# Kernel optimization log

Hardware: AMD Instinct MI355X
Metric: run time of the kernel (lower is better)

The kernel has to match this reference:

```python
import jax, jax.numpy as jnp
import numpy as np

N, DIM, EMB = 8192, 128, 16
WIDTHS = [64, 32, 16]


def setup_inputs() -> dict:
    key = jax.random.key(0)
    ks = jax.random.split(key, 16)
    x = jax.random.normal(ks[0], (N, DIM), dtype=jnp.float32)
    dims = [DIM] + WIDTHS + [EMB]  # 128 -> 64 -> 32 -> 16 -> 16
    params = {}
    for i in range(4):
        fan_in, fan_out = dims[i], dims[i + 1]
        params[f"W{i+1}"] = jax.random.normal(ks[1 + 2 * i], (fan_in, fan_out), dtype=jnp.float32) * (1.0 / np.sqrt(fan_in))
        params[f"b{i+1}"] = jax.random.normal(ks[2 + 2 * i], (fan_out,), dtype=jnp.float32) * 0.01
    return {"x": x, **params}


def _encode(x, W1, b1, W2, b2, W3, b3, W4, b4):
    h = jax.nn.relu(x @ W1 + b1)
    h = jax.nn.relu(h @ W2 + b2)
    h = jax.nn.relu(h @ W3 + b3)
    return h @ W4 + b4  # [N, EMB]


def _tstudent_probs(z):
    # squared euclidean distances via the norm trick (avoids [N,N,EMB] tensor)
    sq = jnp.sum(z * z, axis=1)  # [N]
    dist = jnp.maximum(sq[:, None] + sq[None, :] - 2.0 * (z @ z.T), 0.0)  # [N,N]
    numerator = 1.0 / (1.0 + dist)
    return numerator / jnp.sum(numerator, axis=1, keepdims=True)


def reference(x, W1, b1, W2, b2, W3, b3, W4, b4):
    z = _encode(x, W1, b1, W2, b2, W3, b3, W4, b4)
    return _tstudent_probs(z)
```

## Files before the change

### kernel.cpp

```cpp
#include <hip/hip_runtime.h>

#define N 8192
#define DIM 128
#define NCHUNK 32

__global__ __launch_bounds__(64) void encoder_kernel(
    const float* __restrict__ x,
    const float* __restrict__ W1, const float* __restrict__ b1,
    const float* __restrict__ W2, const float* __restrict__ b2,
    const float* __restrict__ W3, const float* __restrict__ b3,
    const float* __restrict__ W4, const float* __restrict__ b4,
    float* __restrict__ z, float* __restrict__ sqout)
{
    __shared__ float sW2[64 * 32];
    __shared__ float sW3[32 * 16];
    __shared__ float sW4[16 * 16];
    __shared__ float sb1[64];
    __shared__ float sb2[32];
    __shared__ float sb3[16];
    __shared__ float sb4[16];
    __shared__ float sW1[128 * 64];
    __shared__ float sh1[64 * 65];

    int t = threadIdx.x;
    float* sh2 = sW1;
    float* sh3 = sW1 + 2112;

    for (int idx = t; idx < 128 * 64; idx += 64) sW1[idx] = W1[idx];
    for (int idx = t; idx < 64 * 32; idx += 64) sW2[idx] = W2[idx];
    for (int idx = t; idx < 32 * 16; idx += 64) sW3[idx] = W3[idx];
    for (int idx = t; idx < 16 * 16; idx += 64) sW4[idx] = W4[idx];
    sb1[t] = b1[t];
    if (t < 32) sb2[t] = b2[t];
    if (t < 16) { sb3[t] = b3[t]; sb4[t] = b4[t]; }
    __syncthreads();

    int row = blockIdx.x * 64 + t;
    const float4* xr = (const float4*)(x + (size_t)row * DIM);

    float h1[64];
    #pragma unroll
    for (int k = 0; k < 64; ++k) h1[k] = sb1[k];
    for (int j4 = 0; j4 < 32; ++j4) {
        float4 xv = xr[j4];
        const float* w0 = &sW1[(j4 * 4 + 0) * 64];
        const float* w1 = &sW1[(j4 * 4 + 1) * 64];
        const float* w2 = &sW1[(j4 * 4 + 2) * 64];
        const float* w3 = &sW1[(j4 * 4 + 3) * 64];
        #pragma unroll
        for (int k = 0; k < 64; ++k) h1[k] = fmaf(xv.x, w0[k], h1[k]);
        #pragma unroll
        for (int k = 0; k < 64; ++k) h1[k] = fmaf(xv.y, w1[k], h1[k]);
        #pragma unroll
        for (int k = 0; k < 64; ++k) h1[k] = fmaf(xv.z, w2[k], h1[k]);
        #pragma unroll
        for (int k = 0; k < 64; ++k) h1[k] = fmaf(xv.w, w3[k], h1[k]);
    }
    #pragma unroll
    for (int k = 0; k < 64; ++k) sh1[t * 65 + k] = fmaxf(h1[k], 0.0f);

    float h2[32];
    #pragma unroll
    for (int k = 0; k < 32; ++k) h2[k] = sb2[k];
    for (int j = 0; j < 64; ++j) {
        float a = sh1[t * 65 + j];
        #pragma unroll
        for (int k = 0; k < 32; ++k) h2[k] = fmaf(a, sW2[j * 32 + k], h2[k]);
    }
    #pragma unroll
    for (int k = 0; k < 32; ++k) sh2[t * 33 + k] = fmaxf(h2[k], 0.0f);

    float h3[16];
    #pragma unroll
    for (int k = 0; k < 16; ++k) h3[k] = sb3[k];
    for (int j = 0; j < 32; ++j) {
        float a = sh2[t * 33 + j];
        #pragma unroll
        for (int k = 0; k < 16; ++k) h3[k] = fmaf(a, sW3[j * 16 + k], h3[k]);
    }
    #pragma unroll
    for (int k = 0; k < 16; ++k) sh3[t * 17 + k] = fmaxf(h3[k], 0.0f);

    float zo[16];
    #pragma unroll
    for (int k = 0; k < 16; ++k) zo[k] = sb4[k];
    for (int j = 0; j < 16; ++j) {
        float a = sh3[t * 17 + j];
        #pragma unroll
        for (int k = 0; k < 16; ++k) zo[k] = fmaf(a, sW4[j * 16 + k], zo[k]);
    }

    float s = 0.0f;
    #pragma unroll
    for (int k = 0; k < 16; ++k) s = fmaf(zo[k], zo[k], s);
    sqout[row] = s;
    float4* zr = (float4*)(z + (size_t)row * 16);
    zr[0] = make_float4(zo[0], zo[1], zo[2], zo[3]);
    zr[1] = make_float4(zo[4], zo[5], zo[6], zo[7]);
    zr[2] = make_float4(zo[8], zo[9], zo[10], zo[11]);
    zr[3] = make_float4(zo[12], zo[13], zo[14], zo[15]);
}

__global__ __launch_bounds__(256) void pass1_kernel(
    const float* __restrict__ z, const float* __restrict__ sq,
    float* __restrict__ partial)
{
    __shared__ float s_zj[256 * 16];
    __shared__ float s_sqj[256];

    int t = threadIdx.x;
    int i0 = blockIdx.x * 256 + t;
    int i1 = i0 + 4096;
    int jb = blockIdx.y * 256;

    {
        const float4* src = (const float4*)(z + (size_t)(jb + t) * 16);
        float4* dst = (float4*)(s_zj + t * 16);
        dst[0] = src[0]; dst[1] = src[1]; dst[2] = src[2]; dst[3] = src[3];
        s_sqj[t] = sq[jb + t];
    }

    float zi0[16], zi1[16];
    {
        const float4* p0 = (const float4*)(z + (size_t)i0 * 16);
        const float4* p1 = (const float4*)(z + (size_t)i1 * 16);
        #pragma unroll
        for (int q = 0; q < 4; ++q) {
            float4 v0 = p0[q]; float4 v1 = p1[q];
            zi0[4*q] = v0.x; zi0[4*q+1] = v0.y; zi0[4*q+2] = v0.z; zi0[4*q+3] = v0.w;
            zi1[4*q] = v1.x; zi1[4*q+1] = v1.y; zi1[4*q+2] = v1.z; zi1[4*q+3] = v1.w;
        }
    }
    float sqi0 = sq[i0], sqi1 = sq[i1];
    __syncthreads();

    float acc0 = 0.0f, acc1 = 0.0f;
    #pragma unroll 4
    for (int jj = 0; jj < 256; ++jj) {
        const float* zj = s_zj + jj * 16;
        float d0 = 0.0f, d1 = 0.0f;
        #pragma unroll
        for (int k = 0; k < 16; ++k) {
            float w = zj[k];
            d0 = fmaf(zi0[k], w, d0);
            d1 = fmaf(zi1[k], w, d1);
        }
        float sj = s_sqj[jj];
        float dist0 = fmaxf(fmaf(-2.0f, d0, sqi0 + sj), 0.0f);
        float dist1 = fmaxf(fmaf(-2.0f, d1, sqi1 + sj), 0.0f);
        acc0 += __builtin_amdgcn_rcpf(1.0f + dist0);
        acc1 += __builtin_amdgcn_rcpf(1.0f + dist1);
    }
    partial[blockIdx.y * N + i0] = acc0;
    partial[blockIdx.y * N + i1] = acc1;
}

__global__ __launch_bounds__(256) void pass2_kernel(
    const float* __restrict__ z, const float* __restrict__ sq,
    const float* __restrict__ partial, float* __restrict__ out)
{
    __shared__ float s_zi[16 * 16];
    __shared__ float s_sqi[16];
    __shared__ float s_inv[16];
    __shared__ float s_red[16 * NCHUNK];

    int t = threadIdx.x;
    int ibase = blockIdx.x * 16;

    s_zi[t] = z[(size_t)ibase * 16 + t];
    if (t < 16) s_sqi[t] = sq[ibase + t];
    for (int q = t; q < 16 * NCHUNK; q += 256) {
        int ii = q >> 5;
        int c  = q & (NCHUNK - 1);
        s_red[ii * NCHUNK + c] = partial[(size_t)c * N + ibase + ii];
    }
    __syncthreads();
    if (t < 16) {
        float s = 0.0f;
        #pragma unroll
        for (int c = 0; c < NCHUNK; ++c) s += s_red[t * NCHUNK + c];
        s_inv[t] = 1.0f / s;
    }
    __syncthreads();

    for (int jb = 0; jb < N; jb += 256) {
        int j = jb + t;
        float zj[16];
        {
            const float4* zp = (const float4*)(z + (size_t)j * 16);
            #pragma unroll
            for (int q = 0; q < 4; ++q) {
                float4 v = zp[q];
                zj[4*q] = v.x; zj[4*q+1] = v.y; zj[4*q+2] = v.z; zj[4*q+3] = v.w;
            }
        }
        float sqj = sq[j];
        #pragma unroll
        for (int ii = 0; ii < 16; ++ii) {
            const float* zi = s_zi + ii * 16;
            float d = 0.0f;
            #pragma unroll
            for (int k = 0; k < 16; ++k) d = fmaf(zi[k], zj[k], d);
            float dist = fmaxf(fmaf(-2.0f, d, s_sqi[ii] + sqj), 0.0f);
            float num = __builtin_amdgcn_rcpf(1.0f + dist);
            __builtin_nontemporal_store(num * s_inv[ii],
                                        &out[(size_t)(ibase + ii) * N + j]);
        }
    }
}

extern "C" void kernel_launch(void* const* d_in, const int* in_sizes, int n_in,
                              void* d_out, int out_size, void* d_ws, size_t ws_size,
                              hipStream_t stream) {
    const float* x  = (const float*)d_in[0];
    const float* W1 = (const float*)d_in[1];
    const float* b1 = (const float*)d_in[2];
    const float* W2 = (const float*)d_in[3];
    const float* b2 = (const float*)d_in[4];
    const float* W3 = (const float*)d_in[5];
    const float* b3 = (const float*)d_in[6];
    const float* W4 = (const float*)d_in[7];
    const float* b4 = (const float*)d_in[8];
    float* out = (float*)d_out;

    float* ws = (float*)d_ws;
    float* z       = ws;
    float* sq      = ws + N * 16;
    float* partial = ws + N * 16 + N;

    encoder_kernel<<<128, 64, 0, stream>>>(x, W1, b1, W2, b2, W3, b3, W4, b4, z, sq);
    pass1_kernel<<<dim3(16, NCHUNK), 256, 0, stream>>>(z, sq, partial);
    pass2_kernel<<<N / 16, 256, 0, stream>>>(z, sq, partial, out);
}
```

Before: 395.4 us.

## Pack z, norms and inverse row sums into one record and use broadcast reads

The encoder now writes each z row together with its squared norm into a 32-float packed record. A separate reduce kernel stores the inverse row sum into that same record. Pass1 and pass2 drop shared-memory staging: each thread holds one row's vector in registers and loops over the other rows, reading them through wave-uniform broadcast global loads. In pass2 each thread now writes one column across 512 rows, so each store is a coalesced row segment; the price is heavy reliance on cache for the broadcast loads and an extra kernel launch.

```diff
diff --git a/kernel.cpp b/kernel.cpp
--- a/kernel.cpp
+++ b/kernel.cpp
@@ -2,7 +2,8 @@
 
 #define N 8192
 #define DIM 128
-#define NCHUNK 32
+#define PACK 32
+#define P1_JCHUNK 16
 
 __global__ __launch_bounds__(64) void encoder_kernel(
     const float* __restrict__ x,
@@ -10,7 +11,7 @@
     const float* __restrict__ W2, const float* __restrict__ b2,
     const float* __restrict__ W3, const float* __restrict__ b3,
     const float* __restrict__ W4, const float* __restrict__ b4,
-    float* __restrict__ z, float* __restrict__ sqout)
+    float* __restrict__ packed)
 {
     __shared__ float sW2[64 * 32];
     __shared__ float sW3[32 * 16];
@@ -93,119 +94,89 @@
     float s = 0.0f;
     #pragma unroll
     for (int k = 0; k < 16; ++k) s = fmaf(zo[k], zo[k], s);
-    sqout[row] = s;
-    float4* zr = (float4*)(z + (size_t)row * 16);
-    zr[0] = make_float4(zo[0], zo[1], zo[2], zo[3]);
-    zr[1] = make_float4(zo[4], zo[5], zo[6], zo[7]);
-    zr[2] = make_float4(zo[8], zo[9], zo[10], zo[11]);
-    zr[3] = make_float4(zo[12], zo[13], zo[14], zo[15]);
+
+    float* pr = packed + (size_t)row * PACK;
+    float4* pv = (float4*)pr;
+    pv[0] = make_float4(zo[0], zo[1], zo[2], zo[3]);
+    pv[1] = make_float4(zo[4], zo[5], zo[6], zo[7]);
+    pv[2] = make_float4(zo[8], zo[9], zo[10], zo[11]);
+    pv[3] = make_float4(zo[12], zo[13], zo[14], zo[15]);
+    pr[16] = s;
 }
 
 __global__ __launch_bounds__(256) void pass1_kernel(
-    const float* __restrict__ z, const float* __restrict__ sq,
-    float* __restrict__ partial)
-{
-    __shared__ float s_zj[256 * 16];
-    __shared__ float s_sqj[256];
-
+    const float* __restrict__ packed, float* __restrict__ partial)
+{
     int t = threadIdx.x;
-    int i0 = blockIdx.x * 256 + t;
-    int i1 = i0 + 4096;
-    int jb = blockIdx.y * 256;
-
+    int i = blockIdx.x * 256 + t;
+    const int JPB = N / P1_JCHUNK;
+    int jb = blockIdx.y * JPB;
+
+    float zi[16];
+    float sqi;
     {
-        const float4* src = (const float4*)(z + (size_t)(jb + t) * 16);
-        float4* dst = (float4*)(s_zj + t * 16);
-        dst[0] = src[0]; dst[1] = src[1]; dst[2] = src[2]; dst[3] = src[3];
-        s_sqj[t] = sq[jb + t];
-    }
-
-    float zi0[16], zi1[16];
+        const float4* p = (const float4*)(packed + (size_t)i * PACK);
+        #pragma unroll
+        for (int q = 0; q < 4; ++q) {
+            float4 v = p[q];
+            zi[4*q] = v.x; zi[4*q+1] = v.y; zi[4*q+2] = v.z; zi[4*q+3] = v.w;
+        }
+        sqi = packed[(size_t)i * PACK + 16];
+    }
+
+    float acc = 0.0f;
+    const float* pr = packed + (size_t)jb * PACK;
+    #pragma unroll 2
+    for (int j = 0; j < JPB; ++j, pr += PACK) {
+        float d = 0.0f;
+        #pragma unroll
+        for (int k = 0; k < 16; ++k) d = fmaf(pr[k], zi[k], d);
+        float dist = fmaxf(fmaf(-2.0f, d, sqi + pr[16]), 0.0f);
+        acc += __builtin_amdgcn_rcpf(1.0f + dist);
+    }
+    partial[(size_t)blockIdx.y * N + i] = acc;
+}
+
+__global__ __launch_bounds__(256) void reduce_kernel(
+    const float* __restrict__ partial, float* __restrict__ packed)
+{
+    int i = blockIdx.x * 256 + threadIdx.x;
+    float s = 0.0f;
+    #pragma unroll
+    for (int c = 0; c < P1_JCHUNK; ++c) s += partial[(size_t)c * N + i];
+    packed[(size_t)i * PACK + 17] = 1.0f / s;
+}
+
+__global__ __launch_bounds__(256) void pass2_kernel(
+    const float* __restrict__ packed, float* __restrict__ out)
+{
+    int t = threadIdx.x;
+    int j = blockIdx.x * 256 + t;
+    const int IPB = N / 16;
+    int i0 = blockIdx.y * IPB;
+
+    float zj[16];
+    float sqj;
     {
-        const float4* p0 = (const float4*)(z + (size_t)i0 * 16);
-        const float4* p1 = (const float4*)(z + (size_t)i1 * 16);
+        const float4* p = (const float4*)(packed + (size_t)j * PACK);
         #pragma unroll
         for (int q = 0; q < 4; ++q) {
-            float4 v0 = p0[q]; float4 v1 = p1[q];
-            zi0[4*q] = v0.x; zi0[4*q+1] = v0.y; zi0[4*q+2] = v0.z; zi0[4*q+3] = v0.w;
-            zi1[4*q] = v1.x; zi1[4*q+1] = v1.y; zi1[4*q+2] = v1.z; zi1[4*q+3] = v1.w;
+            float4 v = p[q];
+            zj[4*q] = v.x; zj[4*q+1] = v.y; zj[4*q+2] = v.z; zj[4*q+3] = v.w;
         }
-    }
-    float sqi0 = sq[i0], sqi1 = sq[i1];
-    __syncthreads();
-
-    float acc0 = 0.0f, acc1 = 0.0f;
-    #pragma unroll 4
-    for (int jj = 0; jj < 256; ++jj) {
-        const float* zj = s_zj + jj * 16;
-        float d0 = 0.0f, d1 = 0.0f;
-        #pragma unroll
-        for (int k = 0; k < 16; ++k) {
-            float w = zj[k];
-            d0 = fmaf(zi0[k], w, d0);
-            d1 = fmaf(zi1[k], w, d1);
-        }
-        float sj = s_sqj[jj];
-        float dist0 = fmaxf(fmaf(-2.0f, d0, sqi0 + sj), 0.0f);
-        float dist1 = fmaxf(fmaf(-2.0f, d1, sqi1 + sj), 0.0f);
-        acc0 += __builtin_amdgcn_rcpf(1.0f + dist0);
-        acc1 += __builtin_amdgcn_rcpf(1.0f + dist1);
-    }
-    partial[blockIdx.y * N + i0] = acc0;
-    partial[blockIdx.y * N + i1] = acc1;
-}
-
-__global__ __launch_bounds__(256) void pass2_kernel(
-    const float* __restrict__ z, const float* __restrict__ sq,
-    const float* __restrict__ partial, float* __restrict__ out)
-{
-    __shared__ float s_zi[16 * 16];
-    __shared__ float s_sqi[16];
-    __shared__ float s_inv[16];
-    __shared__ float s_red[16 * NCHUNK];
-
-    int t = threadIdx.x;
-    int ibase = blockIdx.x * 16;
-
-    s_zi[t] = z[(size_t)ibase * 16 + t];
-    if (t < 16) s_sqi[t] = sq[ibase + t];
-    for (int q = t; q < 16 * NCHUNK; q += 256) {
-        int ii = q >> 5;
-        int c  = q & (NCHUNK - 1);
-        s_red[ii * NCHUNK + c] = partial[(size_t)c * N + ibase + ii];
-    }
-    __syncthreads();
-    if (t < 16) {
-        float s = 0.0f;
-        #pragma unroll
-        for (int c = 0; c < NCHUNK; ++c) s += s_red[t * NCHUNK + c];
-        s_inv[t] = 1.0f / s;
-    }
-    __syncthreads();
-
-    for (int jb = 0; jb < N; jb += 256) {
-        int j = jb + t;
-        float zj[16];
-        {
-            const float4* zp = (const float4*)(z + (size_t)j * 16);
-            #pragma unroll
-            for (int q = 0; q < 4; ++q) {
-                float4 v = zp[q];
-                zj[4*q] = v.x; zj[4*q+1] = v.y; zj[4*q+2] = v.z; zj[4*q+3] = v.w;
-            }
-        }
-        float sqj = sq[j];
-        #pragma unroll
-        for (int ii = 0; ii < 16; ++ii) {
-            const float* zi = s_zi + ii * 16;
-            float d = 0.0f;
-            #pragma unroll
-            for (int k = 0; k < 16; ++k) d = fmaf(zi[k], zj[k], d);
-            float dist = fmaxf(fmaf(-2.0f, d, s_sqi[ii] + sqj), 0.0f);
-            float num = __builtin_amdgcn_rcpf(1.0f + dist);
-            __builtin_nontemporal_store(num * s_inv[ii],
-                                        &out[(size_t)(ibase + ii) * N + j]);
-        }
+        sqj = packed[(size_t)j * PACK + 16];
+    }
+
+    const float* pr = packed + (size_t)i0 * PACK;
+    float* op = out + (size_t)i0 * N + j;
+    #pragma unroll 2
+    for (int i = 0; i < IPB; ++i, pr += PACK, op += N) {
+        float d = 0.0f;
+        #pragma unroll
+        for (int k = 0; k < 16; ++k) d = fmaf(pr[k], zj[k], d);
+        float dist = fmaxf(fmaf(-2.0f, d, sqj + pr[16]), 0.0f);
+        float num = __builtin_amdgcn_rcpf(1.0f + dist);
+        __builtin_nontemporal_store(num * pr[17], op);
     }
 }
 
@@ -224,11 +195,11 @@
     float* out = (float*)d_out;
 
     float* ws = (float*)d_ws;
-    float* z       = ws;
-    float* sq      = ws + N * 16;
-    float* partial = ws + N * 16 + N;
-
-    encoder_kernel<<<128, 64, 0, stream>>>(x, W1, b1, W2, b2, W3, b3, W4, b4, z, sq);
-    pass1_kernel<<<dim3(16, NCHUNK), 256, 0, stream>>>(z, sq, partial);
-    pass2_kernel<<<N / 16, 256, 0, stream>>>(z, sq, partial, out);
-}
+    float* packed  = ws;
+    float* partial = ws + (size_t)N * PACK;
+
+    encoder_kernel<<<128, 64, 0, stream>>>(x, W1, b1, W2, b2, W3, b3, W4, b4, packed);
+    pass1_kernel<<<dim3(32, P1_JCHUNK), 256, 0, stream>>>(packed, partial);
+    reduce_kernel<<<32, 256, 0, stream>>>(partial, packed);
+    pass2_kernel<<<dim3(32, 16), 256, 0, stream>>>(packed, out);
+}
```

New measurement: 465.9 us. 17.8% more time.
